# Optimization experiments

Hardware: AMD Instinct MI355X
Metric: run time of the kernel (lower is better)

The kernel has to match this reference:

```python
import jax, jax.numpy as jnp
import numpy as np

B, S, D, H, L = 64, 512, 512, 512, 2  # batch, seq_len, input_size, hidden_size, num_layers


def setup_inputs() -> dict:
    key = jax.random.key(0)
    ks = jax.random.split(key, 4)
    s = 0.03  # keep gate pre-activations in the non-saturated range
    x = jax.random.normal(ks[0], (B, S, D), jnp.float32)
    h = jnp.zeros((B, L, H), jnp.float32)
    Wr = jax.random.normal(ks[1], (L, D + H, H), jnp.float32) * s
    Wz = jax.random.normal(ks[2], (L, D + H, H), jnp.float32) * s
    Wh = jax.random.normal(ks[3], (L, D + H, H), jnp.float32) * s
    br = jnp.zeros((L, H), jnp.float32)
    bz = jnp.zeros((L, H), jnp.float32)
    bh = jnp.zeros((L, H), jnp.float32)
    return dict(x=x, h=h, Wr=Wr, br=br, Wz=Wz, bz=bz, Wh=Wh, bh=bh)


def _gru_layer(x, h0, Wr, br, Wz, bz, Wh, bh):
    # Linear(cat(x, h)) == x @ W[:Din] + h @ W[Din:] + b ; precompute the x part
    Din = x.shape[-1]
    gx_r = jnp.einsum('bsd,dh->bsh', x, Wr[:Din]) + br  # [B,S,H]
    gx_z = jnp.einsum('bsd,dh->bsh', x, Wz[:Din]) + bz
    gx_h = jnp.einsum('bsd,dh->bsh', x, Wh[:Din]) + bh
    Wrh, Wzh, Whh = Wr[Din:], Wz[Din:], Wh[Din:]  # [H,H]

    def step(h, gates):
        gr, gz, gh = gates  # each [B,H]
        r = jax.nn.sigmoid(gr + h @ Wrh)
        z = jax.nn.sigmoid(gz + h @ Wzh)
        h_tilde = jnp.tanh(gh + (r * h) @ Whh)
        h = (1.0 - z) * h + z * h_tilde
        return h, h

    hT, ys = jax.lax.scan(
        step, h0,
        (gx_r.swapaxes(0, 1), gx_z.swapaxes(0, 1), gx_h.swapaxes(0, 1)))
    return ys.swapaxes(0, 1), hT  # [B,S,H], [B,H]


def reference(x, h, Wr, br, Wz, bz, Wh, bh):
    inp = x
    finals = []
    for l in range(L):
        inp, hT = _gru_layer(inp, h[:, l], Wr[l], br[l], Wz[l], bz[l], Wh[l], bh[l])
        finals.append(hT)
    return inp, jnp.stack(finals, axis=1)  # y:[B,S,H], final_h:[B,L,H]
```

## Files before the change

kernel.cpp:

```cpp
#include <hip/hip_runtime.h>

typedef unsigned int uint;
typedef unsigned short u16;
typedef short s16x8 __attribute__((ext_vector_type(8)));
typedef float f32x4 __attribute__((ext_vector_type(4)));
typedef uint u32x4 __attribute__((ext_vector_type(4)));

#define MFMA16(a, b, c) __builtin_amdgcn_mfma_f32_16x16x32_bf16((a), (b), (c), 0, 0, 0)

static const size_t OFF_SYNC = 0;
static const size_t OFF_HB   = 2048;
static const size_t OFF_RHB  = 526336;
static const size_t OFF_WT   = 1050624;
static const size_t OFF_YS0  = 7342080;
static const size_t OFF_GX   = 40896512;
static const size_t GX_ELEMS = (size_t)512 * 64 * 1536;

__device__ __forceinline__ short f2bf(float x) {
  uint u = __builtin_bit_cast(uint, x);
  u = u + 0x7fffu + ((u >> 16) & 1u);
  return (short)(u >> 16);
}
__device__ __forceinline__ float bf2f(u16 v) {
  uint u = ((uint)v) << 16;
  return __builtin_bit_cast(float, u);
}

__device__ __forceinline__ u32x4 ld16(const void* p) {
  u32x4 r;
  asm volatile("global_load_dwordx4 %0, %1, off" : "=v"(r) : "v"(p));
  return r;
}
__device__ __forceinline__ uint ld4u(const void* p) {
  uint r;
  asm volatile("global_load_dword %0, %1, off" : "=v"(r) : "v"(p));
  return r;
}
__device__ __forceinline__ uint ld2x(const void* p) {
  uint r;
  asm volatile("global_load_ushort %0, %1, off" : "=v"(r) : "v"(p));
  return r;
}
__device__ __forceinline__ void st4(void* p, uint v) {
  asm volatile("global_store_dword %0, %1, off" :: "v"(p), "v"(v));
}
__device__ __forceinline__ void st2(void* p, u16 v) {
  uint x = v;
  asm volatile("global_store_short %0, %1, off" :: "v"(p), "v"(x));
}
__device__ __forceinline__ u32x4 ld16c(const void* p) {
  u32x4 r;
  asm volatile("global_load_dwordx4 %0, %1, off sc0 sc1" : "=v"(r) : "v"(p));
  return r;
}
__device__ __forceinline__ void st2c(void* p, u16 v) {
  uint x = v;
  asm volatile("global_store_short %0, %1, off sc0 sc1" :: "v"(p), "v"(x));
}
__device__ __forceinline__ void waitv0() {
  asm volatile("s_waitcnt vmcnt(0)" ::: "memory");
  __builtin_amdgcn_sched_barrier(0);
}

template <int GXBF>
__device__ __forceinline__ float upk(uint v) {
  if constexpr (GXBF) return bf2f((u16)v);
  else return __builtin_bit_cast(float, v);
}

__global__ void sentinel_kernel(float* __restrict__ out, float v) {
  out[threadIdx.x] = v;
}

__global__ void init_kernel(const float* __restrict__ h_in, u16* __restrict__ hb,
                            int* __restrict__ sync) {
  int idx = blockIdx.x * 256 + threadIdx.x;
  if (idx < 512) sync[idx] = 0;
  for (int i = idx; i < 2 * 64 * 512; i += gridDim.x * 256) {
    int l = i >> 15, b = (i >> 9) & 63, c = i & 511;
    int q = b >> 4, ob = b & 15;
    hb[((l * 4 + q) * 4 + 0) * 8192 + ob * 512 + c] = (u16)f2bf(h_in[(b * 2 + l) * 512 + c]);
  }
}

__global__ void convert_w_kernel(const float* __restrict__ Wr, const float* __restrict__ Wz,
                                 const float* __restrict__ Wh, u16* __restrict__ WT) {
  int idx = blockIdx.x * 256 + threadIdx.x;
  int n = idx & 511, k = (idx >> 9) & 1023, lg = idx >> 19;
  int l = (lg >= 3) ? 1 : 0, g = lg - l * 3;
  const float* W = (g == 0 ? Wr : (g == 1 ? Wz : Wh)) + (size_t)l * 1024 * 512;
  WT[((size_t)lg * 512 + n) * 1024 + k] = (u16)f2bf(W[k * 512 + n]);
}

template <int GXBF>
__global__ __launch_bounds__(256) void proj_kernel(
    const float* __restrict__ A, const u16* __restrict__ WT,
    const float* __restrict__ br, const float* __restrict__ bz, const float* __restrict__ bh,
    void* __restrict__ gx) {
  __shared__ u16 Alds[128 * 64];
  __shared__ u16 Blds[128 * 64];
  const int tid = threadIdx.x;
  const int wave = tid >> 6, lane = tid & 63;
  const int lan15 = lane & 15, lanhi = lane >> 4;
  const int mb = blockIdx.x & 255, nb = blockIdx.x >> 8;
  const int m0 = mb * 128, n0 = nb * 128;
  const int wm = (wave >> 1) * 64, wn = (wave & 1) * 64;

  const f32x4 z4 = {0.f, 0.f, 0.f, 0.f};
  f32x4 acc[4][4];
#pragma unroll
  for (int i = 0; i < 4; ++i)
#pragma unroll
    for (int j = 0; j < 4; ++j) acc[i][j] = z4;

  for (int kb = 0; kb < 512; kb += 64) {
    __syncthreads();
#pragma unroll
    for (int p = 0; p < 4; ++p) {
      int idx = p * 256 + tid;
      int row = idx >> 3, slot = idx & 7;
      const float* src = A + (size_t)(m0 + row) * 512 + kb + slot * 8;
      float4 v0 = *(const float4*)src;
      float4 v1 = *(const float4*)(src + 4);
      u16 tmp[8] = {(u16)f2bf(v0.x), (u16)f2bf(v0.y), (u16)f2bf(v0.z), (u16)f2bf(v0.w),
                    (u16)f2bf(v1.x), (u16)f2bf(v1.y), (u16)f2bf(v1.z), (u16)f2bf(v1.w)};
      *(uint4*)((char*)Alds + row * 128 + ((slot ^ (row & 7)) * 16)) = *(uint4*)tmp;
    }
#pragma unroll
    for (int p = 0; p < 4; ++p) {
      int idx = p * 256 + tid;
      int row = idx >> 3, slot = idx & 7;
      int ng = n0 + row, g = ng >> 9, nc = ng & 511;
      uint4 v = *(const uint4*)(WT + ((size_t)g * 512 + nc) * 1024 + kb + slot * 8);
      *(uint4*)((char*)Blds + row * 128 + ((slot ^ (row & 7)) * 16)) = v;
    }
    __syncthreads();
#pragma unroll
    for (int ks = 0; ks < 2; ++ks) {
      s16x8 af[4], bfr[4];
#pragma unroll
      for (int f = 0; f < 4; ++f) {
        int rowA = wm + f * 16 + lan15;
        af[f] = *(const s16x8*)((const char*)Alds + rowA * 128 + (((ks * 4 + lanhi) ^ (rowA & 7)) * 16));
        int rowB = wn + f * 16 + lan15;
        bfr[f] = *(const s16x8*)((const char*)Blds + rowB * 128 + (((ks * 4 + lanhi) ^ (rowB & 7)) * 16));
      }
#pragma unroll
      for (int mf = 0; mf < 4; ++mf)
#pragma unroll
        for (int nf = 0; nf < 4; ++nf)
          acc[mf][nf] = MFMA16(af[mf], bfr[nf], acc[mf][nf]);
    }
  }
#pragma unroll
  for (int nf = 0; nf < 4; ++nf) {
    int n = n0 + wn + nf * 16 + lan15;
    int g = n >> 9, nc = n & 511;
    float bias = (g == 0 ? br[nc] : (g == 1 ? bz[nc] : bh[nc]));
#pragma unroll
    for (int mf = 0; mf < 4; ++mf) {
#pragma unroll
      for (int q = 0; q < 4; ++q) {
        int m = m0 + wm + mf * 16 + lanhi * 4 + q;
        int s = m & 511, b = m >> 9;
        size_t e = (size_t)(s * 64 + b) * 1536 + n;
        float v = acc[mf][nf][q] + bias;
        if constexpr (GXBF) ((u16*)gx)[e] = (u16)f2bf(v);
        else ((float*)gx)[e] = v;
      }
    }
  }
}

__device__ __forceinline__ void gbarA(int* bar, int target) {
  asm volatile("s_waitcnt vmcnt(0)" ::: "memory");
  __syncthreads();
  if (threadIdx.x == 0) {
    int one = 1;
    asm volatile("global_atomic_add %0, %1, off" :: "v"(bar), "v"(one) : "memory");
    int v, zero = 0, iter = 0;
    do {
      __builtin_amdgcn_s_sleep(1);
      asm volatile("global_atomic_add %0, %1, %2, off sc0\n\ts_waitcnt vmcnt(0)"
                   : "=v"(v) : "v"(bar), "v"(zero) : "memory");
    } while (v < target && ++iter < (1 << 17));
  }
  __syncthreads();
  __builtin_amdgcn_sched_barrier(0);
}
__device__ __forceinline__ void bar_arrive(int* bar) {
  asm volatile("s_waitcnt vmcnt(0)" ::: "memory");
  __syncthreads();
  if (threadIdx.x == 0) {
    int one = 1;
    asm volatile("global_atomic_add %0, %1, off" :: "v"(bar), "v"(one) : "memory");
  }
}
__device__ __forceinline__ void bar_wait(int* bar, int target) {
  if (threadIdx.x == 0) {
    int v, zero = 0, iter = 0;
    do {
      __builtin_amdgcn_s_sleep(1);
      asm volatile("global_atomic_add %0, %1, %2, off sc0\n\ts_waitcnt vmcnt(0)"
                   : "=v"(v) : "v"(bar), "v"(zero) : "memory");
    } while (v < target && ++iter < (1 << 17));
  }
  __syncthreads();
  __builtin_amdgcn_sched_barrier(0);
}

__device__ __forceinline__ int ROFF(int w, int c, int b) {
  return (w * 48 + c) * 20 + b;
}

template <int GXBF>
__global__ __launch_bounds__(256, 1) void gru_pipe(
    const void* __restrict__ gx,
    const u16* __restrict__ WT,
    const float* __restrict__ h_in,
    u16* __restrict__ hb,
    u16* __restrict__ rhb,
    u16* __restrict__ ys0,
    const float* __restrict__ br, const float* __restrict__ bz, const float* __restrict__ bh,
    float* __restrict__ out_f32,
    float* __restrict__ finals,
    int* __restrict__ sync) {
  __shared__ float red[21504];
  __shared__ int s_pack, s_prog;

  if (threadIdx.x == 0) {
    int xcc;
    asm volatile("s_getreg_b32 %0, hwreg(HW_REG_XCC_ID)" : "=s"(xcc));
    xcc &= 7;
    int slot = __hip_atomic_fetch_add(&sync[256 + xcc], 1, __ATOMIC_RELAXED,
                                      __HIP_MEMORY_SCOPE_AGENT);
    s_pack = slot | (xcc << 8);
    s_prog = 0;
  }
  __syncthreads();
  const int slot = s_pack & 255;
  const int xcc  = s_pack >> 8;
  if (slot >= 32) return;

  const int l = (xcc >> 2) & 1, q = xcc & 3;
  int* bar  = sync + xcc * 32;
  int* prog = sync + 320 + q * 32;

  const int tid = threadIdx.x;
  const int wave = tid >> 6, lane = tid & 63;
  const int lan15 = lane & 15, lanhi = lane >> 4;
  const int c0 = slot * 16;
  const int kw = wave * 128;
  const int ke8 = lanhi * 8;
  const int ob = tid >> 4;
  const int col = c0 + (tid & 15);
  const int gb = q * 16 + ob;
  const int ES = GXBF ? 2 : 4;
  const f32x4 z4 = {0.f, 0.f, 0.f, 0.f};

  const u16* WTl = WT + (size_t)l * 3 * 512 * 1024;
  u16* hbq  = hb  + (size_t)(l * 4 + q) * 4 * 8192;
  u16* rhbq = rhb + (size_t)(l * 4 + q) * 4 * 8192;

  s16x8 wrz[2][4], whh[4];
#pragma unroll
  for (int g = 0; g < 2; ++g)
#pragma unroll
    for (int ks = 0; ks < 4; ++ks)
      wrz[g][ks] = *(const s16x8*)(WTl + ((size_t)(g * 512 + c0 + lan15)) * 1024 + 512 + kw + ks * 32 + ke8);
#pragma unroll
  for (int ks = 0; ks < 4; ++ks)
    whh[ks] = *(const s16x8*)(WTl + ((size_t)(1024 + c0 + lan15)) * 1024 + 512 + kw + ks * 32 + ke8);

  float hown = h_in[(gb * 2 + l) * 512 + col];

  if (l == 0) {
    uint pf_r = 0, pf_z = 0, pf_hn = 0, pf_hc = 0;
    auto issue_pf = [&](int tp) {
      const char* gq = (const char*)gx + ((size_t)(tp * 64 + gb) * 1536 + col) * ES;
      if constexpr (GXBF) {
        pf_r = ld2x(gq); pf_z = ld2x(gq + 512 * 2); pf_hn = ld2x(gq + 1024 * 2);
      } else {
        pf_r = ld4u(gq); pf_z = ld4u(gq + 512 * 4); pf_hn = ld4u(gq + 1024 * 4);
      }
    };
    issue_pf(0);

    int tgt = 0;
    for (int t = 0; t < 512; ++t) {
      const u16* hc = hbq + (t & 3) * 8192;
      u16* rhc = rhbq + (t & 3) * 8192;
      u32x4 hl[4];
#pragma unroll
      for (int ks = 0; ks < 4; ++ks)
        hl[ks] = ld16(hc + lan15 * 512 + kw + ks * 32 + ke8);
      waitv0();
      f32x4 a0 = z4, a1 = z4;
#pragma unroll
      for (int ks = 0; ks < 4; ++ks) {
        s16x8 ah = __builtin_bit_cast(s16x8, hl[ks]);
        a0 = MFMA16(ah, wrz[0][ks], a0);
        a1 = MFMA16(ah, wrz[1][ks], a1);
      }
      *(f32x4*)(red + ROFF(wave, lan15, lanhi * 4)) = a0;
      *(f32x4*)(red + ROFF(wave, 16 + lan15, lanhi * 4)) = a1;
      __syncthreads();
      float zg;
      {
        float rp = upk<GXBF>(pf_r), zp = upk<GXBF>(pf_z);
#pragma unroll
        for (int w = 0; w < 4; ++w) {
          rp += red[ROFF(w, col - c0, ob)];
          zp += red[ROFF(w, 16 + (col - c0), ob)];
        }
        float r = 1.f / (1.f + __expf(-rp));
        zg = 1.f / (1.f + __expf(-zp));
        st2(rhc + ob * 512 + col, (u16)f2bf(r * hown));
      }
      tgt += 32; gbarA(bar, tgt);
      pf_hc = pf_hn;
      u32x4 rl[4];
#pragma unroll
      for (int ks = 0; ks < 4; ++ks)
        rl[ks] = ld16(rhc + lan15 * 512 + kw + ks * 32 + ke8);
      issue_pf(t < 511 ? t + 1 : 511);
      asm volatile("s_waitcnt vmcnt(3)" ::: "memory");
      __builtin_amdgcn_sched_barrier(0);
      f32x4 a2 = z4;
#pragma unroll
      for (int ks = 0; ks < 4; ++ks)
        a2 = MFMA16(__builtin_bit_cast(s16x8, rl[ks]), whh[ks], a2);
      *(f32x4*)(red + ROFF(wave, lan15, lanhi * 4)) = a2;
      __syncthreads();
      float hn;
      {
        float wp = upk<GXBF>(pf_hc);
#pragma unroll
        for (int w = 0; w < 4; ++w) wp += red[ROFF(w, col - c0, ob)];
        float pre = fminf(15.f, fmaxf(-15.f, wp));
        float e = __expf(-2.f * pre);
        float ht = (1.f - e) / (1.f + e);
        hn = (1.f - zg) * hown + zg * ht;
        hown = hn;
        u16 hv = (u16)f2bf(hn);
        st2(hbq + ((t + 1) & 3) * 8192 + ob * 512 + col, hv);
        st2c(ys0 + ((size_t)gb * 512 + t) * 512 + col, hv);
      }
      tgt += 32;
      gbarA(bar, tgt);
      if (tid == 0 && slot == 0)
        __hip_atomic_fetch_add(prog, 1, __ATOMIC_RELAXED, __HIP_MEMORY_SCOPE_AGENT);
      if (t == 511)
        finals[(size_t)(gb * 2 + 0) * 512 + col] = hn;
    }
  } else {
    s16x8 w1rz[2][4], w1h[4];
#pragma unroll
    for (int g = 0; g < 2; ++g)
#pragma unroll
      for (int ks = 0; ks < 4; ++ks)
        w1rz[g][ks] = *(const s16x8*)(WTl + ((size_t)(g * 512 + c0 + lan15)) * 1024 + kw + ks * 32 + ke8);
#pragma unroll
    for (int ks = 0; ks < 4; ++ks)
      w1h[ks] = *(const s16x8*)(WTl + ((size_t)(1024 + c0 + lan15)) * 1024 + kw + ks * 32 + ke8);
    const float brv = br[512 + col], bzv = bz[512 + col], bhv = bh[512 + col];

    u32x4 yl[4];
    if (tid == 0) {
      int pv, it = 0;
      do {
        pv = __hip_atomic_load(prog, __ATOMIC_RELAXED, __HIP_MEMORY_SCOPE_AGENT);
        if (pv > 0) break;
        __builtin_amdgcn_s_sleep(2);
      } while (++it < (1 << 22));
      s_prog = pv;
    }
    __syncthreads();
    __builtin_amdgcn_sched_barrier(0);
#pragma unroll
    for (int ks = 0; ks < 4; ++ks)
      yl[ks] = ld16c(ys0 + ((size_t)(q * 16 + lan15) * 512 + 0) * 512 + kw + ks * 32 + ke8);

    int tgt = 0;
    for (int t = 0; t < 512; ++t) {
      const u16* hc = hbq + (t & 3) * 8192;
      u16* rhc = rhbq + (t & 3) * 8192;
      u32x4 hl[4];
#pragma unroll
      for (int ks = 0; ks < 4; ++ks)
        hl[ks] = ld16(hc + lan15 * 512 + kw + ks * 32 + ke8);
      waitv0();
      f32x4 a0 = z4, a1 = z4, a2 = z4;
#pragma unroll
      for (int ks = 0; ks < 4; ++ks) {
        s16x8 ah = __builtin_bit_cast(s16x8, hl[ks]);
        s16x8 ay = __builtin_bit_cast(s16x8, yl[ks]);
        a0 = MFMA16(ah, wrz[0][ks], a0);
        a0 = MFMA16(ay, w1rz[0][ks], a0);
        a1 = MFMA16(ah, wrz[1][ks], a1);
        a1 = MFMA16(ay, w1rz[1][ks], a1);
        a2 = MFMA16(ay, w1h[ks], a2);
      }
      *(f32x4*)(red + ROFF(wave, lan15, lanhi * 4)) = a0;
      *(f32x4*)(red + ROFF(wave, 16 + lan15, lanhi * 4)) = a1;
      *(f32x4*)(red + ROFF(wave, 32 + lan15, lanhi * 4)) = a2;
      __syncthreads();
      float zg, w1c;
      {
        float rp = brv, zp = bzv, wc = 0.f;
#pragma unroll
        for (int w = 0; w < 4; ++w) {
          rp += red[ROFF(w, col - c0, ob)];
          zp += red[ROFF(w, 16 + (col - c0), ob)];
          wc += red[ROFF(w, 32 + (col - c0), ob)];
        }
        float r = 1.f / (1.f + __expf(-rp));
        zg = 1.f / (1.f + __expf(-zp));
        w1c = wc;
        st2(rhc + ob * 512 + col, (u16)f2bf(r * hown));
      }
      tgt += 32;
      bar_arrive(bar);
      if (t != 511) {
        if (s_prog < t + 2) {
          if (tid == 0) {
            int pv, it = 0;
            do {
              pv = __hip_atomic_load(prog, __ATOMIC_RELAXED, __HIP_MEMORY_SCOPE_AGENT);
              if (pv >= t + 2) break;
              __builtin_amdgcn_s_sleep(2);
            } while (++it < (1 << 22));
            s_prog = pv;
          }
          __syncthreads();
        }
#pragma unroll
        for (int ks = 0; ks < 4; ++ks)
          yl[ks] = ld16c(ys0 + ((size_t)(q * 16 + lan15) * 512 + (t + 1)) * 512 + kw + ks * 32 + ke8);
      }
      bar_wait(bar, tgt);
      u32x4 rl[4];
#pragma unroll
      for (int ks = 0; ks < 4; ++ks)
        rl[ks] = ld16(rhc + lan15 * 512 + kw + ks * 32 + ke8);
      waitv0();
      f32x4 a3 = z4;
#pragma unroll
      for (int ks = 0; ks < 4; ++ks)
        a3 = MFMA16(__builtin_bit_cast(s16x8, rl[ks]), whh[ks], a3);
      *(f32x4*)(red + ROFF(wave, lan15, lanhi * 4)) = a3;
      __syncthreads();
      float hn;
      {
        float wp = bhv + w1c;
#pragma unroll
        for (int w = 0; w < 4; ++w) wp += red[ROFF(w, col - c0, ob)];
        float pre = fminf(15.f, fmaxf(-15.f, wp));
        float e = __expf(-2.f * pre);
        float ht = (1.f - e) / (1.f + e);
        hn = (1.f - zg) * hown + zg * ht;
        hown = hn;
        st2(hbq + ((t + 1) & 3) * 8192 + ob * 512 + col, (u16)f2bf(hn));
      }
      tgt += 32;
      if (t != 511) {
        bar_arrive(bar);
        st4(out_f32 + ((size_t)gb * 512 + t) * 512 + col, __builtin_bit_cast(uint, hn));
        bar_wait(bar, tgt);
      } else {
        st4(out_f32 + ((size_t)gb * 512 + t) * 512 + col, __builtin_bit_cast(uint, hn));
        finals[(size_t)(gb * 2 + 1) * 512 + col] = hn;
      }
    }
  }
}

template <int GXBF>
static void run_all(const float* x, const float* h, const float* Wr, const float* br,
                    const float* Wz, const float* bz, const float* Wh, const float* bh,
                    float* out, char* ws, hipStream_t stream) {
  int* sync  = (int*)(ws + OFF_SYNC);
  u16* hbAll = (u16*)(ws + OFF_HB);
  u16* rhb   = (u16*)(ws + OFF_RHB);
  u16* WT    = (u16*)(ws + OFF_WT);
  u16* ys0   = (u16*)(ws + OFF_YS0);
  void* gx   = (void*)(ws + OFF_GX);
  float* finals = out + 16777216;

  init_kernel<<<64, 256, 0, stream>>>(h, hbAll, sync);
  convert_w_kernel<<<12288, 256, 0, stream>>>(Wr, Wz, Wh, WT);
  proj_kernel<GXBF><<<3072, 256, 0, stream>>>(x, WT, br, bz, bh, gx);
  gru_pipe<GXBF><<<256, 256, 0, stream>>>(gx, WT, h, hbAll, rhb, ys0,
                                          br, bz, bh, out, finals, sync);
}

extern "C" void kernel_launch(void* const* d_in, const int* in_sizes, int n_in,
                              void* d_out, int out_size, void* d_ws, size_t ws_size,
                              hipStream_t stream) {
  const float* x  = (const float*)d_in[0];
  const float* h  = (const float*)d_in[1];
  const float* Wr = (const float*)d_in[2];
  const float* br = (const float*)d_in[3];
  const float* Wz = (const float*)d_in[4];
  const float* bz = (const float*)d_in[5];
  const float* Wh = (const float*)d_in[6];
  const float* bh = (const float*)d_in[7];
  float* out = (float*)d_out;
  char* ws = (char*)d_ws;

  const size_t need_f32 = OFF_GX + GX_ELEMS * 4;
  const size_t need_bf  = OFF_GX + GX_ELEMS * 2;

  if (ws_size >= need_f32) {
    run_all<0>(x, h, Wr, br, Wz, bz, Wh, bh, out, ws, stream);
  } else if (ws_size >= need_bf) {
    run_all<1>(x, h, Wr, br, Wz, bz, Wh, bh, out, ws, stream);
  } else {
    sentinel_kernel<<<1, 64, 0, stream>>>(out, (float)ws_size);
  }
}
```

Measured before the change: 2.423 ms.

## Halve recurrent workgroups per XCC by giving each block 32 hidden columns

Each persistent GRU block now owns 32 hidden columns instead of 16, so only 16 blocks per XCC take part in the per-step grid barrier instead of 32. Each block does twice the MFMA work per step with doubled weight registers and a larger LDS reduction buffer. The barrier spin loops now check the counter before sleeping, which removes a sleep from the fast path. The sync area and workspace offsets are enlarged and zeroed to match. The aim is to cut barrier latency and atomic contention on the serial critical path, at the cost of more per-block compute and register pressure.

After: 2.359 ms. -2.6%, faster.

```diff
diff --git a/kernel.cpp b/kernel.cpp
--- a/kernel.cpp
+++ b/kernel.cpp
@@ -9,11 +9,11 @@
 #define MFMA16(a, b, c) __builtin_amdgcn_mfma_f32_16x16x32_bf16((a), (b), (c), 0, 0, 0)
 
 static const size_t OFF_SYNC = 0;
-static const size_t OFF_HB   = 2048;
-static const size_t OFF_RHB  = 526336;
-static const size_t OFF_WT   = 1050624;
-static const size_t OFF_YS0  = 7342080;
-static const size_t OFF_GX   = 40896512;
+static const size_t OFF_HB   = 36864;
+static const size_t OFF_RHB  = 561152;
+static const size_t OFF_WT   = 1085440;
+static const size_t OFF_YS0  = 7376896;
+static const size_t OFF_GX   = 40931328;
 static const size_t GX_ELEMS = (size_t)512 * 64 * 1536;
 
 __device__ __forceinline__ short f2bf(float x) {
@@ -75,7 +75,7 @@
 __global__ void init_kernel(const float* __restrict__ h_in, u16* __restrict__ hb,
                             int* __restrict__ sync) {
   int idx = blockIdx.x * 256 + threadIdx.x;
-  if (idx < 512) sync[idx] = 0;
+  if (idx < 8704) sync[idx] = 0;
   for (int i = idx; i < 2 * 64 * 512; i += gridDim.x * 256) {
     int l = i >> 15, b = (i >> 9) & 63, c = i & 511;
     int q = b >> 4, ob = b & 15;
@@ -180,10 +180,11 @@
     asm volatile("global_atomic_add %0, %1, off" :: "v"(bar), "v"(one) : "memory");
     int v, zero = 0, iter = 0;
     do {
-      __builtin_amdgcn_s_sleep(1);
       asm volatile("global_atomic_add %0, %1, %2, off sc0\n\ts_waitcnt vmcnt(0)"
                    : "=v"(v) : "v"(bar), "v"(zero) : "memory");
-    } while (v < target && ++iter < (1 << 17));
+      if (v >= target) break;
+      __builtin_amdgcn_s_sleep(1);
+    } while (++iter < (1 << 17));
   }
   __syncthreads();
   __builtin_amdgcn_sched_barrier(0);
@@ -200,17 +201,18 @@
   if (threadIdx.x == 0) {
     int v, zero = 0, iter = 0;
     do {
-      __builtin_amdgcn_s_sleep(1);
       asm volatile("global_atomic_add %0, %1, %2, off sc0\n\ts_waitcnt vmcnt(0)"
                    : "=v"(v) : "v"(bar), "v"(zero) : "memory");
-    } while (v < target && ++iter < (1 << 17));
+      if (v >= target) break;
+      __builtin_amdgcn_s_sleep(1);
+    } while (++iter < (1 << 17));
   }
   __syncthreads();
   __builtin_amdgcn_sched_barrier(0);
 }
 
 __device__ __forceinline__ int ROFF(int w, int c, int b) {
-  return (w * 48 + c) * 20 + b;
+  return (w * 96 + c) * 20 + b;
 }
 
 template <int GXBF>
@@ -240,7 +242,7 @@
   __syncthreads();
   const int slot = s_pack & 255;
   const int xcc  = s_pack >> 8;
-  if (slot >= 32) return;
+  if (slot >= 16) return;
 
   const int l = (xcc >> 2) & 1, q = xcc & 3;
   int* bar  = sync + xcc * 32;
@@ -249,11 +251,12 @@
   const int tid = threadIdx.x;
   const int wave = tid >> 6, lane = tid & 63;
   const int lan15 = lane & 15, lanhi = lane >> 4;
-  const int c0 = slot * 16;
+  const int c0 = slot * 32;
   const int kw = wave * 128;
   const int ke8 = lanhi * 8;
   const int ob = tid >> 4;
-  const int col = c0 + (tid & 15);
+  const int ci = tid & 15;
+  const int col0 = c0 + ci, col1 = c0 + 16 + ci;
   const int gb = q * 16 + ob;
   const int ES = GXBF ? 2 : 4;
   const f32x4 z4 = {0.f, 0.f, 0.f, 0.f};
@@ -262,31 +265,39 @@
   u16* hbq  = hb  + (size_t)(l * 4 + q) * 4 * 8192;
   u16* rhbq = rhb + (size_t)(l * 4 + q) * 4 * 8192;
 
-  s16x8 wrz[2][4], whh[4];
+  s16x8 wrz[2][2][4], whh[2][4];
 #pragma unroll
   for (int g = 0; g < 2; ++g)
 #pragma unroll
+    for (int j = 0; j < 2; ++j)
+#pragma unroll
+      for (int ks = 0; ks < 4; ++ks)
+        wrz[g][j][ks] = *(const s16x8*)(WTl + ((size_t)(g * 512 + c0 + j * 16 + lan15)) * 1024 + 512 + kw + ks * 32 + ke8);
+#pragma unroll
+  for (int j = 0; j < 2; ++j)
+#pragma unroll
     for (int ks = 0; ks < 4; ++ks)
-      wrz[g][ks] = *(const s16x8*)(WTl + ((size_t)(g * 512 + c0 + lan15)) * 1024 + 512 + kw + ks * 32 + ke8);
-#pragma unroll
-  for (int ks = 0; ks < 4; ++ks)
-    whh[ks] = *(const s16x8*)(WTl + ((size_t)(1024 + c0 + lan15)) * 1024 + 512 + kw + ks * 32 + ke8);
-
-  float hown = h_in[(gb * 2 + l) * 512 + col];
+      whh[j][ks] = *(const s16x8*)(WTl + ((size_t)(1024 + c0 + j * 16 + lan15)) * 1024 + 512 + kw + ks * 32 + ke8);
+
+  float hown0 = h_in[(gb * 2 + l) * 512 + col0];
+  float hown1 = h_in[(gb * 2 + l) * 512 + col1];
 
   if (l == 0) {
-    uint pf_r = 0, pf_z = 0, pf_hn = 0, pf_hc = 0;
+    uint pf_r0 = 0, pf_r1 = 0, pf_z0 = 0, pf_z1 = 0, pf_hn0 = 0, pf_hn1 = 0, pf_hc0 = 0, pf_hc1 = 0;
     auto issue_pf = [&](int tp) {
-      const char* gq = (const char*)gx + ((size_t)(tp * 64 + gb) * 1536 + col) * ES;
+      const char* gq = (const char*)gx + ((size_t)(tp * 64 + gb) * 1536 + col0) * ES;
       if constexpr (GXBF) {
-        pf_r = ld2x(gq); pf_z = ld2x(gq + 512 * 2); pf_hn = ld2x(gq + 1024 * 2);
+        pf_r0 = ld2x(gq);            pf_r1 = ld2x(gq + 32);
+        pf_z0 = ld2x(gq + 1024);     pf_z1 = ld2x(gq + 1056);
+        pf_hn0 = ld2x(gq + 2048);    pf_hn1 = ld2x(gq + 2080);
       } else {
-        pf_r = ld4u(gq); pf_z = ld4u(gq + 512 * 4); pf_hn = ld4u(gq + 1024 * 4);
+        pf_r0 = ld4u(gq);            pf_r1 = ld4u(gq + 64);
+        pf_z0 = ld4u(gq + 2048);     pf_z1 = ld4u(gq + 2112);
+        pf_hn0 = ld4u(gq + 4096);    pf_hn1 = ld4u(gq + 4160);
       }
     };
     issue_pf(0);
 
-    int tgt = 0;
     for (int t = 0; t < 512; ++t) {
       const u16* hc = hbq + (t & 3) * 8192;
       u16* rhc = rhbq + (t & 3) * 8192;
@@ -295,75 +306,103 @@
       for (int ks = 0; ks < 4; ++ks)
         hl[ks] = ld16(hc + lan15 * 512 + kw + ks * 32 + ke8);
       waitv0();
-      f32x4 a0 = z4, a1 = z4;
+      f32x4 ar0 = z4, ar1 = z4, az0 = z4, az1 = z4;
 #pragma unroll
       for (int ks = 0; ks < 4; ++ks) {
         s16x8 ah = __builtin_bit_cast(s16x8, hl[ks]);
-        a0 = MFMA16(ah, wrz[0][ks], a0);
-        a1 = MFMA16(ah, wrz[1][ks], a1);
-      }
-      *(f32x4*)(red + ROFF(wave, lan15, lanhi * 4)) = a0;
-      *(f32x4*)(red + ROFF(wave, 16 + lan15, lanhi * 4)) = a1;
+        ar0 = MFMA16(ah, wrz[0][0][ks], ar0);
+        ar1 = MFMA16(ah, wrz[0][1][ks], ar1);
+        az0 = MFMA16(ah, wrz[1][0][ks], az0);
+        az1 = MFMA16(ah, wrz[1][1][ks], az1);
+      }
+      *(f32x4*)(red + ROFF(wave, lan15, lanhi * 4)) = ar0;
+      *(f32x4*)(red + ROFF(wave, 16 + lan15, lanhi * 4)) = ar1;
+      *(f32x4*)(red + ROFF(wave, 32 + lan15, lanhi * 4)) = az0;
+      *(f32x4*)(red + ROFF(wave, 48 + lan15, lanhi * 4)) = az1;
       __syncthreads();
-      float zg;
+      float zg0, zg1;
       {
-        float rp = upk<GXBF>(pf_r), zp = upk<GXBF>(pf_z);
+        float rp0 = upk<GXBF>(pf_r0), zp0 = upk<GXBF>(pf_z0);
+        float rp1 = upk<GXBF>(pf_r1), zp1 = upk<GXBF>(pf_z1);
 #pragma unroll
         for (int w = 0; w < 4; ++w) {
-          rp += red[ROFF(w, col - c0, ob)];
-          zp += red[ROFF(w, 16 + (col - c0), ob)];
+          rp0 += red[ROFF(w, ci, ob)];
+          rp1 += red[ROFF(w, 16 + ci, ob)];
+          zp0 += red[ROFF(w, 32 + ci, ob)];
+          zp1 += red[ROFF(w, 48 + ci, ob)];
         }
-        float r = 1.f / (1.f + __expf(-rp));
-        zg = 1.f / (1.f + __expf(-zp));
-        st2(rhc + ob * 512 + col, (u16)f2bf(r * hown));
-      }
-      tgt += 32; gbarA(bar, tgt);
-      pf_hc = pf_hn;
+        float r0 = 1.f / (1.f + __expf(-rp0));
+        float r1 = 1.f / (1.f + __expf(-rp1));
+        zg0 = 1.f / (1.f + __expf(-zp0));
+        zg1 = 1.f / (1.f + __expf(-zp1));
+        st2(rhc + ob * 512 + col0, (u16)f2bf(r0 * hown0));
+        st2(rhc + ob * 512 + col1, (u16)f2bf(r1 * hown1));
+      }
+      gbarA(bar, 16 * (2 * t + 1));
+      pf_hc0 = pf_hn0; pf_hc1 = pf_hn1;
       u32x4 rl[4];
 #pragma unroll
       for (int ks = 0; ks < 4; ++ks)
         rl[ks] = ld16(rhc + lan15 * 512 + kw + ks * 32 + ke8);
       issue_pf(t < 511 ? t + 1 : 511);
-      asm volatile("s_waitcnt vmcnt(3)" ::: "memory");
+      asm volatile("s_waitcnt vmcnt(6)" ::: "memory");
       __builtin_amdgcn_sched_barrier(0);
-      f32x4 a2 = z4;
-#pragma unroll
-      for (int ks = 0; ks < 4; ++ks)
-        a2 = MFMA16(__builtin_bit_cast(s16x8, rl[ks]), whh[ks], a2);
-      *(f32x4*)(red + ROFF(wave, lan15, lanhi * 4)) = a2;
+      f32x4 ah0 = z4, ah1 = z4;
+#pragma unroll
+      for (int ks = 0; ks < 4; ++ks) {
+        s16x8 av = __builtin_bit_cast(s16x8, rl[ks]);
+        ah0 = MFMA16(av, whh[0][ks], ah0);
+        ah1 = MFMA16(av, whh[1][ks], ah1);
+      }
+      *(f32x4*)(red + ROFF(wave, lan15, lanhi * 4)) = ah0;
+      *(f32x4*)(red + ROFF(wave, 16 + lan15, lanhi * 4)) = ah1;
       __syncthreads();
-      float hn;
+      float hn0, hn1;
       {
-        float wp = upk<GXBF>(pf_hc);
-#pragma unroll
-        for (int w = 0; w < 4; ++w) wp += red[ROFF(w, col - c0, ob)];
-        float pre = fminf(15.f, fmaxf(-15.f, wp));
-        float e = __expf(-2.f * pre);
-        float ht = (1.f - e) / (1.f + e);
-        hn = (1.f - zg) * hown + zg * ht;
-        hown = hn;
-        u16 hv = (u16)f2bf(hn);
-        st2(hbq + ((t + 1) & 3) * 8192 + ob * 512 + col, hv);
-        st2c(ys0 + ((size_t)gb * 512 + t) * 512 + col, hv);
-      }
-      tgt += 32;
-      gbarA(bar, tgt);
+        float wp0 = upk<GXBF>(pf_hc0), wp1 = upk<GXBF>(pf_hc1);
+#pragma unroll
+        for (int w = 0; w < 4; ++w) {
+          wp0 += red[ROFF(w, ci, ob)];
+          wp1 += red[ROFF(w, 16 + ci, ob)];
+        }
+        float p0 = fminf(15.f, fmaxf(-15.f, wp0));
+        float p1 = fminf(15.f, fmaxf(-15.f, wp1));
+        float e0 = __expf(-2.f * p0), e1 = __expf(-2.f * p1);
+        float t0 = (1.f - e0) / (1.f + e0), t1 = (1.f - e1) / (1.f + e1);
+        hn0 = (1.f - zg0) * hown0 + zg0 * t0;
+        hn1 = (1.f - zg1) * hown1 + zg1 * t1;
+        hown0 = hn0; hown1 = hn1;
+        u16 hv0 = (u16)f2bf(hn0), hv1 = (u16)f2bf(hn1);
+        u16* hnx = hbq + ((t + 1) & 3) * 8192 + ob * 512;
+        st2(hnx + col0, hv0);
+        st2(hnx + col1, hv1);
+        st2c(ys0 + ((size_t)gb * 512 + t) * 512 + col0, hv0);
+        st2c(ys0 + ((size_t)gb * 512 + t) * 512 + col1, hv1);
+      }
+      gbarA(bar, 16 * (2 * t + 2));
       if (tid == 0 && slot == 0)
         __hip_atomic_fetch_add(prog, 1, __ATOMIC_RELAXED, __HIP_MEMORY_SCOPE_AGENT);
-      if (t == 511)
-        finals[(size_t)(gb * 2 + 0) * 512 + col] = hn;
+      if (t == 511) {
+        finals[(size_t)(gb * 2 + 0) * 512 + col0] = hn0;
+        finals[(size_t)(gb * 2 + 0) * 512 + col1] = hn1;
+      }
     }
   } else {
-    s16x8 w1rz[2][4], w1h[4];
+    s16x8 w1rz[2][2][4], w1h[2][4];
 #pragma unroll
     for (int g = 0; g < 2; ++g)
 #pragma unroll
+      for (int j = 0; j < 2; ++j)
+#pragma unroll
+        for (int ks = 0; ks < 4; ++ks)
+          w1rz[g][j][ks] = *(const s16x8*)(WTl + ((size_t)(g * 512 + c0 + j * 16 + lan15)) * 1024 + kw + ks * 32 + ke8);
+#pragma unroll
+    for (int j = 0; j < 2; ++j)
+#pragma unroll
       for (int ks = 0; ks < 4; ++ks)
-        w1rz[g][ks] = *(const s16x8*)(WTl + ((size_t)(g * 512 + c0 + lan15)) * 1024 + kw + ks * 32 + ke8);
-#pragma unroll
-    for (int ks = 0; ks < 4; ++ks)
-      w1h[ks] = *(const s16x8*)(WTl + ((size_t)(1024 + c0 + lan15)) * 1024 + kw + ks * 32 + ke8);
-    const float brv = br[512 + col], bzv = bz[512 + col], bhv = bh[512 + col];
+        w1h[j][ks] = *(const s16x8*)(WTl + ((size_t)(1024 + c0 + j * 16 + lan15)) * 1024 + kw + ks * 32 + ke8);
+    const float brv0 = br[512 + col0], bzv0 = bz[512 + col0], bhv0 = bh[512 + col0];
+    const float brv1 = br[512 + col1], bzv1 = bz[512 + col1], bhv1 = bh[512 + col1];
 
     u32x4 yl[4];
     if (tid == 0) {
@@ -381,7 +420,6 @@
     for (int ks = 0; ks < 4; ++ks)
       yl[ks] = ld16c(ys0 + ((size_t)(q * 16 + lan15) * 512 + 0) * 512 + kw + ks * 32 + ke8);
 
-    int tgt = 0;
     for (int t = 0; t < 512; ++t) {
       const u16* hc = hbq + (t & 3) * 8192;
       u16* rhc = rhbq + (t & 3) * 8192;
@@ -390,36 +428,50 @@
       for (int ks = 0; ks < 4; ++ks)
         hl[ks] = ld16(hc + lan15 * 512 + kw + ks * 32 + ke8);
       waitv0();
-      f32x4 a0 = z4, a1 = z4, a2 = z4;
+      f32x4 ar0 = z4, ar1 = z4, az0 = z4, az1 = z4, aw0 = z4, aw1 = z4;
 #pragma unroll
       for (int ks = 0; ks < 4; ++ks) {
         s16x8 ah = __builtin_bit_cast(s16x8, hl[ks]);
         s16x8 ay = __builtin_bit_cast(s16x8, yl[ks]);
-        a0 = MFMA16(ah, wrz[0][ks], a0);
-        a0 = MFMA16(ay, w1rz[0][ks], a0);
-        a1 = MFMA16(ah, wrz[1][ks], a1);
-        a1 = MFMA16(ay, w1rz[1][ks], a1);
-        a2 = MFMA16(ay, w1h[ks], a2);
-      }
-      *(f32x4*)(red + ROFF(wave, lan15, lanhi * 4)) = a0;
-      *(f32x4*)(red + ROFF(wave, 16 + lan15, lanhi * 4)) = a1;
-      *(f32x4*)(red + ROFF(wave, 32 + lan15, lanhi * 4)) = a2;
+        ar0 = MFMA16(ah, wrz[0][0][ks], ar0);
+        ar0 = MFMA16(ay, w1rz[0][0][ks], ar0);
+        ar1 = MFMA16(ah, wrz[0][1][ks], ar1);
+        ar1 = MFMA16(ay, w1rz[0][1][ks], ar1);
+        az0 = MFMA16(ah, wrz[1][0][ks], az0);
+        az0 = MFMA16(ay, w1rz[1][0][ks], az0);
+        az1 = MFMA16(ah, wrz[1][1][ks], az1);
+        az1 = MFMA16(ay, w1rz[1][1][ks], az1);
+        aw0 = MFMA16(ay, w1h[0][ks], aw0);
+        aw1 = MFMA16(ay, w1h[1][ks], aw1);
+      }
+      *(f32x4*)(red + ROFF(wave, lan15, lanhi * 4)) = ar0;
+      *(f32x4*)(red + ROFF(wave, 16 + lan15, lanhi * 4)) = ar1;
+      *(f32x4*)(red + ROFF(wave, 32 + lan15, lanhi * 4)) = az0;
+      *(f32x4*)(red + ROFF(wave, 48 + lan15, lanhi * 4)) = az1;
+      *(f32x4*)(red + ROFF(wave, 64 + lan15, lanhi * 4)) = aw0;
+      *(f32x4*)(red + ROFF(wave, 80 + lan15, lanhi * 4)) = aw1;
       __syncthreads();
-      float zg, w1c;
+      float zg0, zg1, w1c0, w1c1;
       {
-        float rp = brv, zp = bzv, wc = 0.f;
+        float rp0 = brv0, zp0 = bzv0, wc0 = 0.f;
+        float rp1 = brv1, zp1 = bzv1, wc1 = 0.f;
 #pragma unroll
         for (int w = 0; w < 4; ++w) {
-          rp += red[ROFF(w, col - c0, ob)];
-          zp += red[ROFF(w, 16 + (col - c0), ob)];
-          wc += red[ROFF(w, 32 + (col - c0), ob)];
+          rp0 += red[ROFF(w, ci, ob)];
+          rp1 += red[ROFF(w, 16 + ci, ob)];
+          zp0 += red[ROFF(w, 32 + ci, ob)];
+          zp1 += red[ROFF(w, 48 + ci, ob)];
+          wc0 += red[ROFF(w, 64 + ci, ob)];
+          wc1 += red[ROFF(w, 80 + ci, ob)];
         }
-        float r = 1.f / (1.f + __expf(-rp));
-        zg = 1.f / (1.f + __expf(-zp));
-        w1c = wc;
-        st2(rhc + ob * 512 + col, (u16)f2bf(r * hown));
-      }
-      tgt += 32;
+        float r0 = 1.f / (1.f + __expf(-rp0));
+        float r1 = 1.f / (1.f + __expf(-rp1));
+        zg0 = 1.f / (1.f + __expf(-zp0));
+        zg1 = 1.f / (1.f + __expf(-zp1));
+        w1c0 = wc0; w1c1 = wc1;
+        st2(rhc + ob * 512 + col0, (u16)f2bf(r0 * hown0));
+        st2(rhc + ob * 512 + col1, (u16)f2bf(r1 * hown1));
+      }
       bar_arrive(bar);
       if (t != 511) {
         if (s_prog < t + 2) {
@@ -438,38 +490,51 @@
         for (int ks = 0; ks < 4; ++ks)
           yl[ks] = ld16c(ys0 + ((size_t)(q * 16 + lan15) * 512 + (t + 1)) * 512 + kw + ks * 32 + ke8);
       }
-      bar_wait(bar, tgt);
+      bar_wait(bar, 16 * (2 * t + 1));
       u32x4 rl[4];
 #pragma unroll
       for (int ks = 0; ks < 4; ++ks)
         rl[ks] = ld16(rhc + lan15 * 512 + kw + ks * 32 + ke8);
       waitv0();
-      f32x4 a3 = z4;
-#pragma unroll
-      for (int ks = 0; ks < 4; ++ks)
-        a3 = MFMA16(__builtin_bit_cast(s16x8, rl[ks]), whh[ks], a3);
-      *(f32x4*)(red + ROFF(wave, lan15, lanhi * 4)) = a3;
+      f32x4 ah0 = z4, ah1 = z4;
+#pragma unroll
+      for (int ks = 0; ks < 4; ++ks) {
+        s16x8 av = __builtin_bit_cast(s16x8, rl[ks]);
+        ah0 = MFMA16(av, whh[0][ks], ah0);
+        ah1 = MFMA16(av, whh[1][ks], ah1);
+      }
+      *(f32x4*)(red + ROFF(wave, lan15, lanhi * 4)) = ah0;
+      *(f32x4*)(red + ROFF(wave, 16 + lan15, lanhi * 4)) = ah1;
       __syncthreads();
-      float hn;
+      float hn0, hn1;
       {
-        float wp = bhv + w1c;
-#pragma unroll
-        for (int w = 0; w < 4; ++w) wp += red[ROFF(w, col - c0, ob)];
-        float pre = fminf(15.f, fmaxf(-15.f, wp));
-        float e = __expf(-2.f * pre);
-        float ht = (1.f - e) / (1.f + e);
-        hn = (1.f - zg) * hown + zg * ht;
-        hown = hn;
-        st2(hbq + ((t + 1) & 3) * 8192 + ob * 512 + col, (u16)f2bf(hn));
-      }
-      tgt += 32;
+        float wp0 = bhv0 + w1c0, wp1 = bhv1 + w1c1;
+#pragma unroll
+        for (int w = 0; w < 4; ++w) {
+          wp0 += red[ROFF(w, ci, ob)];
+          wp1 += red[ROFF(w, 16 + ci, ob)];
+        }
+        float p0 = fminf(15.f, fmaxf(-15.f, wp0));
+        float p1 = fminf(15.f, fmaxf(-15.f, wp1));
+        float e0 = __expf(-2.f * p0), e1 = __expf(-2.f * p1);
+        float t0 = (1.f - e0) / (1.f + e0), t1 = (1.f - e1) / (1.f + e1);
+        hn0 = (1.f - zg0) * hown0 + zg0 * t0;
+        hn1 = (1.f - zg1) * hown1 + zg1 * t1;
+        hown0 = hn0; hown1 = hn1;
+        u16* hnx = hbq + ((t + 1) & 3) * 8192 + ob * 512;
+        st2(hnx + col0, (u16)f2bf(hn0));
+        st2(hnx + col1, (u16)f2bf(hn1));
+      }
       if (t != 511) {
         bar_arrive(bar);
-        st4(out_f32 + ((size_t)gb * 512 + t) * 512 + col, __builtin_bit_cast(uint, hn));
-        bar_wait(bar, tgt);
+        st4(out_f32 + ((size_t)gb * 512 + t) * 512 + col0, __builtin_bit_cast(uint, hn0));
+        st4(out_f32 + ((size_t)gb * 512 + t) * 512 + col1, __builtin_bit_cast(uint, hn1));
+        bar_wait(bar, 16 * (2 * t + 2));
       } else {
-        st4(out_f32 + ((size_t)gb * 512 + t) * 512 + col, __builtin_bit_cast(uint, hn));
-        finals[(size_t)(gb * 2 + 1) * 512 + col] = hn;
+        st4(out_f32 + ((size_t)gb * 512 + t) * 512 + col0, __builtin_bit_cast(uint, hn0));
+        st4(out_f32 + ((size_t)gb * 512 + t) * 512 + col1, __builtin_bit_cast(uint, hn1));
+        finals[(size_t)(gb * 2 + 1) * 512 + col0] = hn0;
+        finals[(size_t)(gb * 2 + 1) * 512 + col1] = hn1;
       }
     }
   }
```
